# Kernel tuning notes

Hardware: AMD Instinct MI355X
Metric: run time of the kernel (lower is better)

## Reference

```python
import jax, jax.numpy as jnp
import numpy as np


def _fake_quant(x, scale, qmin, qmax):
    # per-tensor int8 fake quant: scale -> round -> clamp -> dequant
    q = jnp.clip(jnp.round(x / scale), qmin, qmax)
    return q * scale


def setup_inputs() -> dict:
    key = jax.random.key(0)
    k1, k2, k3 = jax.random.split(key, 3)
    B, IN, OUT = 4096, 2048, 8192
    x = jax.random.normal(k1, (B, IN), dtype=jnp.float32)
    weight = jax.random.normal(k2, (OUT, IN), dtype=jnp.float32) * 0.02
    bias = jax.random.normal(k3, (OUT,), dtype=jnp.float32) * 0.01
    mul_val = jnp.full((1,), 200.0, dtype=jnp.float32)
    return {"x": x, "weight": weight, "bias": bias, "mul_val": mul_val}


def reference(x, weight, bias, mul_val):
    # Int8ActPerTensorFloat: signed, non-narrow range [-128, 127]
    act_scale = jnp.max(jnp.abs(x)) / 128.0
    xq = _fake_quant(x, act_scale, -128.0, 127.0)
    # Int8WeightPerTensorFloat: signed, narrow range [-127, 127]
    w_scale = jnp.max(jnp.abs(weight)) / 127.0
    wq = _fake_quant(weight, w_scale, -127.0, 127.0)
    # linear: y = xq @ wq.T + b, then elementwise scalar multiply
    y = jnp.einsum("bi,oi->bo", xq, wq) + bias
    return mul_val * y
```

## Files before the change

### kernel.cpp

```cpp
#include <hip/hip_runtime.h>


typedef int v4i  __attribute__((ext_vector_type(4)));
typedef int v16i __attribute__((ext_vector_type(16)));

#define MDIM 4096
#define NDIM 8192
#define KDIM 2048
#define NT   (KDIM / 64)

typedef __attribute__((address_space(1))) void* gas_ptr;
typedef __attribute__((address_space(3))) void* las_ptr;

#define XBLK 1024

__global__ __launch_bounds__(256) void absmax2(const float4* __restrict__ x,
                                               const float4* __restrict__ w,
                                               float* __restrict__ partial) {
    const int tid = threadIdx.x;
    const bool isx = blockIdx.x < XBLK;
    float m0 = 0.0f, m1 = 0.0f;
    if (isx) {
        const size_t base = (size_t)blockIdx.x * 256 + tid;
#pragma unroll
        for (int j = 0; j < 8; j += 2) {
            float4 v0 = x[base + (size_t)j * 262144];
            float4 v1 = x[base + (size_t)(j + 1) * 262144];
            m0 = fmaxf(m0, fmaxf(fmaxf(fabsf(v0.x), fabsf(v0.y)),
                                 fmaxf(fabsf(v0.z), fabsf(v0.w))));
            m1 = fmaxf(m1, fmaxf(fmaxf(fabsf(v1.x), fabsf(v1.y)),
                                 fmaxf(fabsf(v1.z), fabsf(v1.w))));
        }
    } else {
        const size_t base = (size_t)(blockIdx.x - XBLK) * 256 + tid;
#pragma unroll
        for (int j = 0; j < 8; j += 2) {
            float4 v0 = w[base + (size_t)j * 524288];
            float4 v1 = w[base + (size_t)(j + 1) * 524288];
            m0 = fmaxf(m0, fmaxf(fmaxf(fabsf(v0.x), fabsf(v0.y)),
                                 fmaxf(fabsf(v0.z), fabsf(v0.w))));
            m1 = fmaxf(m1, fmaxf(fmaxf(fabsf(v1.x), fabsf(v1.y)),
                                 fmaxf(fabsf(v1.z), fabsf(v1.w))));
        }
    }
    float m = fmaxf(m0, m1);
#pragma unroll
    for (int off = 32; off > 0; off >>= 1)
        m = fmaxf(m, __shfl_xor(m, off, 64));
    __shared__ float wm[4];
    if ((tid & 63) == 0) wm[tid >> 6] = m;
    __syncthreads();
    if (tid == 0)
        partial[blockIdx.x] = fmaxf(fmaxf(wm[0], wm[1]), fmaxf(wm[2], wm[3]));
}

__global__ __launch_bounds__(256) void quant2(const float4* __restrict__ x,
                                              v4i* __restrict__ qxp,
                                              const float4* __restrict__ w,
                                              v4i* __restrict__ qwp,
                                              const float* __restrict__ partial,
                                              unsigned* __restrict__ scales) {
    const int tid = threadIdx.x;
    float gx = 0.0f, gw = 0.0f;
#pragma unroll
    for (int j = 0; j < 4; ++j) gx = fmaxf(gx, partial[tid + j * 256]);
#pragma unroll
    for (int j = 0; j < 8; ++j) gw = fmaxf(gw, partial[XBLK + tid + j * 256]);
#pragma unroll
    for (int off = 32; off > 0; off >>= 1) {
        gx = fmaxf(gx, __shfl_xor(gx, off, 64));
        gw = fmaxf(gw, __shfl_xor(gw, off, 64));
    }
    __shared__ float smx[4], smw[4];
    if ((tid & 63) == 0) { smx[tid >> 6] = gx; smw[tid >> 6] = gw; }
    __syncthreads();
    const float fmx = fmaxf(fmaxf(smx[0], smx[1]), fmaxf(smx[2], smx[3]));
    const float fmw = fmaxf(fmaxf(smw[0], smw[1]), fmaxf(smw[2], smw[3]));
    if (blockIdx.x == 0 && tid == 0) {
        scales[0] = __float_as_uint(fmx);
        scales[1] = __float_as_uint(fmw);
    }
    const float sxs = fmx / 128.0f;
    const float sws = fmw / 127.0f;

    const bool isx = blockIdx.x < XBLK;
    const float4* in = isx ? x : w;
    v4i* outp = isx ? qxp : qwp;
    const int total = isx ? (MDIM * KDIM / 16) : (NDIM * KDIM / 16);
    const int nb = isx ? XBLK : (3072 - XBLK);
    const int b  = isx ? blockIdx.x : (blockIdx.x - XBLK);
    const float s  = isx ? sxs : sws;
    const float lo = isx ? -128.0f : -127.0f;
    for (int idx = b * 256 + tid; idx < total; idx += nb * 256) {
        const int c   = idx & 3;
        const int r   = (idx >> 2) & 255;
        const int kt  = (idx >> 10) & 31;
        const int blk = idx >> 15;
        const float4* src = in + (size_t)(blk * 256 + r) * (KDIM / 4) + kt * 16 + c * 4;
        int q[4];
#pragma unroll
        for (int j = 0; j < 4; ++j) {
            float4 v = src[j];
            int b0 = (int)fminf(fmaxf(rintf(v.x / s), lo), 127.0f);
            int b1 = (int)fminf(fmaxf(rintf(v.y / s), lo), 127.0f);
            int b2 = (int)fminf(fmaxf(rintf(v.z / s), lo), 127.0f);
            int b3 = (int)fminf(fmaxf(rintf(v.w / s), lo), 127.0f);
            q[j] = (b0 & 255) | ((b1 & 255) << 8) | ((b2 & 255) << 16) | (b3 << 24);
        }
        v4i qq; qq[0] = q[0]; qq[1] = q[1]; qq[2] = q[2]; qq[3] = q[3];
        outp[((size_t)(blk * 32 + kt) * 4 + c) * 256 + r] = qq;
    }
}

__global__ __launch_bounds__(512, 2) void gemm_i8(
    const signed char* __restrict__ qxp, const signed char* __restrict__ qwp,
    const float* __restrict__ bias, const float* __restrict__ mulv,
    const unsigned* __restrict__ scales, float* __restrict__ out) {
    __shared__ signed char ldsA[4][16384];
    __shared__ signed char ldsB[4][16384];

    const int t    = threadIdx.x;
    const int lane = t & 63;
    const int ln   = lane & 31;
    const int hi   = lane >> 5;
    const int w    = t >> 6;
    const int wr   = w >> 2;
    const int wc   = w & 3;

    const int orig = blockIdx.x;
    const int xcd  = orig & 7;
    const int idx  = orig >> 3;
    const int bm   = (xcd & 1) * 8 + (idx >> 3);
    const int bn   = (xcd >> 1) * 8 + (idx & 7);

    const signed char* srcA = qxp + (size_t)bm * (32 * 16384);
    const signed char* srcB = qwp + (size_t)bn * (32 * 16384);
    signed char* dA = &ldsA[0][0] + t * 16;
    signed char* dB = &ldsB[0][0] + t * 16;

    auto stage = [&](int buf, int kt) {
        const signed char* sa = srcA + kt * 16384 + t * 16;
        const signed char* sb = srcB + kt * 16384 + t * 16;
        __builtin_amdgcn_global_load_lds((gas_ptr)sa,          (las_ptr)(dA + buf * 16384),        16, 0, 0);
        __builtin_amdgcn_global_load_lds((gas_ptr)(sa + 8192), (las_ptr)(dA + buf * 16384 + 8192), 16, 0, 0);
        __builtin_amdgcn_global_load_lds((gas_ptr)sb,          (las_ptr)(dB + buf * 16384),        16, 0, 0);
        __builtin_amdgcn_global_load_lds((gas_ptr)(sb + 8192), (las_ptr)(dB + buf * 16384 + 8192), 16, 0, 0);
    };

    const int aOff = (wr * 128 + ln) * 16;
    const int bOff = (wc * 64  + ln) * 16;

    v16i acc[4][2];
#pragma unroll
    for (int mt = 0; mt < 4; ++mt)
#pragma unroll
        for (int nt = 0; nt < 2; ++nt)
#pragma unroll
            for (int r = 0; r < 16; ++r) acc[mt][nt][r] = 0;

    auto phase = [&](int kt, int stageKt) {
        const int buf = kt & 3;
        const signed char* A0 = &ldsA[buf][0] + hi * 4096;
        const signed char* B0 = &ldsB[buf][0] + hi * 4096;
        const signed char* A1 = &ldsA[buf][0] + (2 + hi) * 4096;
        const signed char* B1 = &ldsB[buf][0] + (2 + hi) * 4096;

        v4i a0[4], a1[4], b0[2], b1[2];
#pragma unroll
        for (int mt = 0; mt < 4; ++mt) a0[mt] = *(const v4i*)(A0 + aOff + mt * 512);
#pragma unroll
        for (int nt = 0; nt < 2; ++nt) b0[nt] = *(const v4i*)(B0 + bOff + nt * 512);
#pragma unroll
        for (int mt = 0; mt < 4; ++mt) a1[mt] = *(const v4i*)(A1 + aOff + mt * 512);
#pragma unroll
        for (int nt = 0; nt < 2; ++nt) b1[nt] = *(const v4i*)(B1 + bOff + nt * 512);

        if (stageKt < NT) stage(stageKt & 3, stageKt);
        __builtin_amdgcn_s_barrier();
        __builtin_amdgcn_s_setprio(1);
#pragma unroll
        for (int mt = 0; mt < 4; ++mt)
#pragma unroll
            for (int nt = 0; nt < 2; ++nt)
                acc[mt][nt] = __builtin_amdgcn_mfma_i32_32x32x32_i8(
                    a0[mt], b0[nt], acc[mt][nt], 0, 0, 0);
#pragma unroll
        for (int mt = 0; mt < 4; ++mt)
#pragma unroll
            for (int nt = 0; nt < 2; ++nt)
                acc[mt][nt] = __builtin_amdgcn_mfma_i32_32x32x32_i8(
                    a1[mt], b1[nt], acc[mt][nt], 0, 0, 0);
        __builtin_amdgcn_s_setprio(0);
    };

    stage(0, 0);
    stage(1, 1);
    stage(2, 2);
    asm volatile("s_waitcnt vmcnt(4)" ::: "memory");
    __builtin_amdgcn_s_barrier();

    for (int j = 0; j < 15; ++j) {
        phase(2 * j, 2 * j + 3);
        __builtin_amdgcn_s_barrier();
        phase(2 * j + 1, 2 * j + 4);
        asm volatile("s_waitcnt vmcnt(4)" ::: "memory");
        __builtin_amdgcn_s_barrier();
    }
    phase(30, NT);
    asm volatile("s_waitcnt vmcnt(0)" ::: "memory");
    __builtin_amdgcn_s_barrier();
    phase(31, NT);

    const float fm = mulv[0];
    const float fs = fm * (__uint_as_float(scales[0]) / 128.0f)
                        * (__uint_as_float(scales[1]) / 127.0f);
    const int colb = bn * 256 + wc * 64 + ln;
    const int hi4  = hi * 4;
#pragma unroll
    for (int nt = 0; nt < 2; ++nt) {
        const int ocol = colb + nt * 32;
        const float bv = bias[ocol] * fm;
#pragma unroll
        for (int mt = 0; mt < 4; ++mt) {
            float* op = out + (size_t)(bm * 256 + wr * 128 + mt * 32) * NDIM + ocol;
#pragma unroll
            for (int r = 0; r < 16; ++r) {
                const int row = (r & 3) + 8 * (r >> 2) + hi4;
                __builtin_nontemporal_store(fs * (float)acc[mt][nt][r] + bv,
                                            op + (size_t)row * NDIM);
            }
        }
    }
}

extern "C" void kernel_launch(void* const* d_in, const int* in_sizes, int n_in,
                              void* d_out, int out_size, void* d_ws, size_t ws_size,
                              hipStream_t stream) {
    const float4* x    = (const float4*)d_in[0];
    const float4* wgt  = (const float4*)d_in[1];
    const float*  bias = (const float*)d_in[2];
    const float*  mulv = (const float*)d_in[3];
    float* out = (float*)d_out;

    unsigned* scales  = (unsigned*)d_ws;
    float*    partial = (float*)((char*)d_ws + 256);
    signed char* qxp  = (signed char*)d_ws + 256 + 16384;
    signed char* qwp  = qxp + (size_t)MDIM * KDIM;

    absmax2<<<3072, 256, 0, stream>>>(x, wgt, partial);
    quant2<<<3072, 256, 0, stream>>>(x, (v4i*)qxp, wgt, (v4i*)qwp,
                                     partial, scales);
    gemm_i8<<<512, 512, 0, stream>>>(qxp, qwp, bias, mulv, scales, out);
}
```

Before: 122.3 us.

## Double-buffer LDS fragment reads in registers to overlap with MFMA

Restructures the int8 GEMM main loop so the LDS fragment reads for the next k-tile are issued before the MFMAs of the current tile, using two register fragment sets in ping-pong fashion. This also removes the mid-phase barrier, so each k-tile now has one barrier instead of two. The aim is to hide LDS read latency behind matrix-core work and cut synchronisation stalls. The cost is higher VGPR pressure from the extra 12 v4i fragments, which could lower occupancy or cause spills, and it relies on the vmcnt/barrier ordering still protecting the buffer reuse.

```diff
diff --git a/kernel.cpp b/kernel.cpp
--- a/kernel.cpp
+++ b/kernel.cpp
@@ -138,7 +138,9 @@
     signed char* dA = &ldsA[0][0] + t * 16;
     signed char* dB = &ldsB[0][0] + t * 16;
 
-    auto stage = [&](int buf, int kt) {
+    auto stage = [&](int kt) {
+        if (kt >= NT) return;
+        const int buf = kt & 3;
         const signed char* sa = srcA + kt * 16384 + t * 16;
         const signed char* sb = srcB + kt * 16384 + t * 16;
         __builtin_amdgcn_global_load_lds((gas_ptr)sa,          (las_ptr)(dA + buf * 16384),        16, 0, 0);
@@ -150,6 +152,42 @@
     const int aOff = (wr * 128 + ln) * 16;
     const int bOff = (wc * 64  + ln) * 16;
 
+#define READ12(A0, B0, A1, B1, KT) do {                                       \
+        const signed char* _Ab = &ldsA[(KT) & 3][0];                          \
+        const signed char* _Bb = &ldsB[(KT) & 3][0];                          \
+        const signed char* _A0 = _Ab + hi * 4096 + aOff;                      \
+        const signed char* _B0 = _Bb + hi * 4096 + bOff;                      \
+        const signed char* _A1 = _Ab + (2 + hi) * 4096 + aOff;                \
+        const signed char* _B1 = _Bb + (2 + hi) * 4096 + bOff;                \
+        A0[0] = *(const v4i*)(_A0);        A0[1] = *(const v4i*)(_A0 + 512);  \
+        A0[2] = *(const v4i*)(_A0 + 1024); A0[3] = *(const v4i*)(_A0 + 1536); \
+        B0[0] = *(const v4i*)(_B0);        B0[1] = *(const v4i*)(_B0 + 512);  \
+        A1[0] = *(const v4i*)(_A1);        A1[1] = *(const v4i*)(_A1 + 512);  \
+        A1[2] = *(const v4i*)(_A1 + 1024); A1[3] = *(const v4i*)(_A1 + 1536); \
+        B1[0] = *(const v4i*)(_B1);        B1[1] = *(const v4i*)(_B1 + 512);  \
+    } while (0)
+
+#define MFMA16(A0, B0, A1, B1) do {                                           \
+        __builtin_amdgcn_s_setprio(1);                                        \
+        acc[0][0] = __builtin_amdgcn_mfma_i32_32x32x32_i8(A0[0], B0[0], acc[0][0], 0, 0, 0); \
+        acc[0][1] = __builtin_amdgcn_mfma_i32_32x32x32_i8(A0[0], B0[1], acc[0][1], 0, 0, 0); \
+        acc[1][0] = __builtin_amdgcn_mfma_i32_32x32x32_i8(A0[1], B0[0], acc[1][0], 0, 0, 0); \
+        acc[1][1] = __builtin_amdgcn_mfma_i32_32x32x32_i8(A0[1], B0[1], acc[1][1], 0, 0, 0); \
+        acc[2][0] = __builtin_amdgcn_mfma_i32_32x32x32_i8(A0[2], B0[0], acc[2][0], 0, 0, 0); \
+        acc[2][1] = __builtin_amdgcn_mfma_i32_32x32x32_i8(A0[2], B0[1], acc[2][1], 0, 0, 0); \
+        acc[3][0] = __builtin_amdgcn_mfma_i32_32x32x32_i8(A0[3], B0[0], acc[3][0], 0, 0, 0); \
+        acc[3][1] = __builtin_amdgcn_mfma_i32_32x32x32_i8(A0[3], B0[1], acc[3][1], 0, 0, 0); \
+        acc[0][0] = __builtin_amdgcn_mfma_i32_32x32x32_i8(A1[0], B1[0], acc[0][0], 0, 0, 0); \
+        acc[0][1] = __builtin_amdgcn_mfma_i32_32x32x32_i8(A1[0], B1[1], acc[0][1], 0, 0, 0); \
+        acc[1][0] = __builtin_amdgcn_mfma_i32_32x32x32_i8(A1[1], B1[0], acc[1][0], 0, 0, 0); \
+        acc[1][1] = __builtin_amdgcn_mfma_i32_32x32x32_i8(A1[1], B1[1], acc[1][1], 0, 0, 0); \
+        acc[2][0] = __builtin_amdgcn_mfma_i32_32x32x32_i8(A1[2], B1[0], acc[2][0], 0, 0, 0); \
+        acc[2][1] = __builtin_amdgcn_mfma_i32_32x32x32_i8(A1[2], B1[1], acc[2][1], 0, 0, 0); \
+        acc[3][0] = __builtin_amdgcn_mfma_i32_32x32x32_i8(A1[3], B1[0], acc[3][0], 0, 0, 0); \
+        acc[3][1] = __builtin_amdgcn_mfma_i32_32x32x32_i8(A1[3], B1[1], acc[3][1], 0, 0, 0); \
+        __builtin_amdgcn_s_setprio(0);                                        \
+    } while (0)
+
     v16i acc[4][2];
 #pragma unroll
     for (int mt = 0; mt < 4; ++mt)
@@ -158,58 +196,31 @@
 #pragma unroll
             for (int r = 0; r < 16; ++r) acc[mt][nt][r] = 0;
 
-    auto phase = [&](int kt, int stageKt) {
-        const int buf = kt & 3;
-        const signed char* A0 = &ldsA[buf][0] + hi * 4096;
-        const signed char* B0 = &ldsB[buf][0] + hi * 4096;
-        const signed char* A1 = &ldsA[buf][0] + (2 + hi) * 4096;
-        const signed char* B1 = &ldsB[buf][0] + (2 + hi) * 4096;
-
-        v4i a0[4], a1[4], b0[2], b1[2];
-#pragma unroll
-        for (int mt = 0; mt < 4; ++mt) a0[mt] = *(const v4i*)(A0 + aOff + mt * 512);
-#pragma unroll
-        for (int nt = 0; nt < 2; ++nt) b0[nt] = *(const v4i*)(B0 + bOff + nt * 512);
-#pragma unroll
-        for (int mt = 0; mt < 4; ++mt) a1[mt] = *(const v4i*)(A1 + aOff + mt * 512);
-#pragma unroll
-        for (int nt = 0; nt < 2; ++nt) b1[nt] = *(const v4i*)(B1 + bOff + nt * 512);
-
-        if (stageKt < NT) stage(stageKt & 3, stageKt);
-        __builtin_amdgcn_s_barrier();
-        __builtin_amdgcn_s_setprio(1);
-#pragma unroll
-        for (int mt = 0; mt < 4; ++mt)
-#pragma unroll
-            for (int nt = 0; nt < 2; ++nt)
-                acc[mt][nt] = __builtin_amdgcn_mfma_i32_32x32x32_i8(
-                    a0[mt], b0[nt], acc[mt][nt], 0, 0, 0);
-#pragma unroll
-        for (int mt = 0; mt < 4; ++mt)
-#pragma unroll
-            for (int nt = 0; nt < 2; ++nt)
-                acc[mt][nt] = __builtin_amdgcn_mfma_i32_32x32x32_i8(
-                    a1[mt], b1[nt], acc[mt][nt], 0, 0, 0);
-        __builtin_amdgcn_s_setprio(0);
-    };
-
-    stage(0, 0);
-    stage(1, 1);
-    stage(2, 2);
+    v4i f0A0[4], f0B0[2], f0A1[4], f0B1[2];
+    v4i f1A0[4], f1B0[2], f1A1[4], f1B1[2];
+
+    stage(0); stage(1); stage(2);
     asm volatile("s_waitcnt vmcnt(4)" ::: "memory");
     __builtin_amdgcn_s_barrier();
+    READ12(f0A0, f0B0, f0A1, f0B1, 0);
 
     for (int j = 0; j < 15; ++j) {
-        phase(2 * j, 2 * j + 3);
-        __builtin_amdgcn_s_barrier();
-        phase(2 * j + 1, 2 * j + 4);
+        const int kt0 = 2 * j;
+        stage(kt0 + 3);
+        READ12(f1A0, f1B0, f1A1, f1B1, kt0 + 1);
+        MFMA16(f0A0, f0B0, f0A1, f0B1);
         asm volatile("s_waitcnt vmcnt(4)" ::: "memory");
         __builtin_amdgcn_s_barrier();
-    }
-    phase(30, NT);
-    asm volatile("s_waitcnt vmcnt(0)" ::: "memory");
-    __builtin_amdgcn_s_barrier();
-    phase(31, NT);
+        stage(kt0 + 4);
+        READ12(f0A0, f0B0, f0A1, f0B1, kt0 + 2);
+        MFMA16(f1A0, f1B0, f1A1, f1B1);
+        if (j < 14) asm volatile("s_waitcnt vmcnt(4)" ::: "memory");
+        else        asm volatile("s_waitcnt vmcnt(0)" ::: "memory");
+        __builtin_amdgcn_s_barrier();
+    }
+    READ12(f1A0, f1B0, f1A1, f1B1, 31);
+    MFMA16(f0A0, f0B0, f0A1, f0B1);
+    MFMA16(f1A0, f1B0, f1A1, f1B1);
 
     const float fm = mulv[0];
     const float fs = fm * (__uint_as_float(scales[0]) / 128.0f)
@@ -231,6 +242,8 @@
             }
         }
     }
+#undef READ12
+#undef MFMA16
 }
 
 extern "C" void kernel_launch(void* const* d_in, const int* in_sizes, int n_in,
```

Measured after the change: 123.2 us. About the same (+0.7%).

## Shrink GEMM tile to 128x256 with 4 waves and triple-buffered LDS

Applied to the files above, without the earlier changes.

The int8 GEMM moves from 256x256 tiles with 8 waves and a 4-deep LDS ring to 128x256 tiles with 4 waves and a 3-deep ring. The grid grows from 512 to 1024 blocks. The activation pre-pack layout changes to 128-row panels to match. The intent is better load balance across CUs and more resident blocks per CU, since each block uses less LDS. The cost is that every B tile is reloaded twice as often, so arithmetic intensity per byte of LDS traffic drops.

```diff
diff --git a/kernel.cpp b/kernel.cpp
--- a/kernel.cpp
+++ b/kernel.cpp
@@ -92,11 +92,23 @@
     const float s  = isx ? sxs : sws;
     const float lo = isx ? -128.0f : -127.0f;
     for (int idx = b * 256 + tid; idx < total; idx += nb * 256) {
-        const int c   = idx & 3;
-        const int r   = (idx >> 2) & 255;
-        const int kt  = (idx >> 10) & 31;
-        const int blk = idx >> 15;
-        const float4* src = in + (size_t)(blk * 256 + r) * (KDIM / 4) + kt * 16 + c * 4;
+        int c, r, kt, blk, row, oidx;
+        if (isx) {
+            c   = idx & 3;
+            r   = (idx >> 2) & 127;
+            kt  = (idx >> 9) & 31;
+            blk = idx >> 14;
+            row = blk * 128 + r;
+            oidx = ((blk * 32 + kt) * 4 + c) * 128 + r;
+        } else {
+            c   = idx & 3;
+            r   = (idx >> 2) & 255;
+            kt  = (idx >> 10) & 31;
+            blk = idx >> 15;
+            row = blk * 256 + r;
+            oidx = ((blk * 32 + kt) * 4 + c) * 256 + r;
+        }
+        const float4* src = in + (size_t)row * (KDIM / 4) + kt * 16 + c * 4;
         int q[4];
 #pragma unroll
         for (int j = 0; j < 4; ++j) {
@@ -108,47 +120,49 @@
             q[j] = (b0 & 255) | ((b1 & 255) << 8) | ((b2 & 255) << 16) | (b3 << 24);
         }
         v4i qq; qq[0] = q[0]; qq[1] = q[1]; qq[2] = q[2]; qq[3] = q[3];
-        outp[((size_t)(blk * 32 + kt) * 4 + c) * 256 + r] = qq;
-    }
-}
-
-__global__ __launch_bounds__(512, 2) void gemm_i8(
+        outp[oidx] = qq;
+    }
+}
+
+__global__ __launch_bounds__(256, 2) void gemm_i8(
     const signed char* __restrict__ qxp, const signed char* __restrict__ qwp,
     const float* __restrict__ bias, const float* __restrict__ mulv,
     const unsigned* __restrict__ scales, float* __restrict__ out) {
-    __shared__ signed char ldsA[4][16384];
-    __shared__ signed char ldsB[4][16384];
+    __shared__ signed char ldsA[3][8192];
+    __shared__ signed char ldsB[3][16384];
 
     const int t    = threadIdx.x;
     const int lane = t & 63;
     const int ln   = lane & 31;
     const int hi   = lane >> 5;
-    const int w    = t >> 6;
-    const int wr   = w >> 2;
-    const int wc   = w & 3;
+    const int wc   = t >> 6;
 
     const int orig = blockIdx.x;
     const int xcd  = orig & 7;
     const int idx  = orig >> 3;
-    const int bm   = (xcd & 1) * 8 + (idx >> 3);
+    const int bm   = (xcd & 1) * 16 + (idx >> 3);
     const int bn   = (xcd >> 1) * 8 + (idx & 7);
 
-    const signed char* srcA = qxp + (size_t)bm * (32 * 16384);
+    const signed char* srcA = qxp + (size_t)bm * (32 * 8192);
     const signed char* srcB = qwp + (size_t)bn * (32 * 16384);
-    signed char* dA = &ldsA[0][0] + t * 16;
-    signed char* dB = &ldsB[0][0] + t * 16;
-
-    auto stage = [&](int buf, int kt) {
-        const signed char* sa = srcA + kt * 16384 + t * 16;
+    signed char* dA0 = &ldsA[0][0] + t * 16;
+    signed char* dB0 = &ldsB[0][0] + t * 16;
+
+    auto stage = [&](int kt, int buf) {
+        const signed char* sa = srcA + kt * 8192  + t * 16;
         const signed char* sb = srcB + kt * 16384 + t * 16;
-        __builtin_amdgcn_global_load_lds((gas_ptr)sa,          (las_ptr)(dA + buf * 16384),        16, 0, 0);
-        __builtin_amdgcn_global_load_lds((gas_ptr)(sa + 8192), (las_ptr)(dA + buf * 16384 + 8192), 16, 0, 0);
-        __builtin_amdgcn_global_load_lds((gas_ptr)sb,          (las_ptr)(dB + buf * 16384),        16, 0, 0);
-        __builtin_amdgcn_global_load_lds((gas_ptr)(sb + 8192), (las_ptr)(dB + buf * 16384 + 8192), 16, 0, 0);
+        signed char* da = dA0 + buf * 8192;
+        signed char* db = dB0 + buf * 16384;
+        __builtin_amdgcn_global_load_lds((gas_ptr)sa,           (las_ptr)da,            16, 0, 0);
+        __builtin_amdgcn_global_load_lds((gas_ptr)(sa + 4096),  (las_ptr)(da + 4096),   16, 0, 0);
+        __builtin_amdgcn_global_load_lds((gas_ptr)sb,           (las_ptr)db,            16, 0, 0);
+        __builtin_amdgcn_global_load_lds((gas_ptr)(sb + 4096),  (las_ptr)(db + 4096),   16, 0, 0);
+        __builtin_amdgcn_global_load_lds((gas_ptr)(sb + 8192),  (las_ptr)(db + 8192),   16, 0, 0);
+        __builtin_amdgcn_global_load_lds((gas_ptr)(sb + 12288), (las_ptr)(db + 12288),  16, 0, 0);
     };
 
-    const int aOff = (wr * 128 + ln) * 16;
-    const int bOff = (wc * 64  + ln) * 16;
+    const int aOff = ln * 16;
+    const int bOff = (wc * 64 + ln) * 16;
 
     v16i acc[4][2];
 #pragma unroll
@@ -158,25 +172,29 @@
 #pragma unroll
             for (int r = 0; r < 16; ++r) acc[mt][nt][r] = 0;
 
-    auto phase = [&](int kt, int stageKt) {
-        const int buf = kt & 3;
-        const signed char* A0 = &ldsA[buf][0] + hi * 4096;
-        const signed char* B0 = &ldsB[buf][0] + hi * 4096;
-        const signed char* A1 = &ldsA[buf][0] + (2 + hi) * 4096;
-        const signed char* B1 = &ldsB[buf][0] + (2 + hi) * 4096;
+    stage(0, 0);
+    stage(1, 1);
+    asm volatile("s_waitcnt vmcnt(6)" ::: "memory");
+    __builtin_amdgcn_s_barrier();
+
+    int cur = 0, stg = 2;
+    for (int kt = 0; kt < NT; ++kt) {
+        const signed char* Ab = &ldsA[cur][0];
+        const signed char* Bb = &ldsB[cur][0];
 
         v4i a0[4], a1[4], b0[2], b1[2];
 #pragma unroll
-        for (int mt = 0; mt < 4; ++mt) a0[mt] = *(const v4i*)(A0 + aOff + mt * 512);
-#pragma unroll
-        for (int nt = 0; nt < 2; ++nt) b0[nt] = *(const v4i*)(B0 + bOff + nt * 512);
-#pragma unroll
-        for (int mt = 0; mt < 4; ++mt) a1[mt] = *(const v4i*)(A1 + aOff + mt * 512);
-#pragma unroll
-        for (int nt = 0; nt < 2; ++nt) b1[nt] = *(const v4i*)(B1 + bOff + nt * 512);
-
-        if (stageKt < NT) stage(stageKt & 3, stageKt);
+        for (int mt = 0; mt < 4; ++mt) a0[mt] = *(const v4i*)(Ab + hi * 2048 + aOff + mt * 512);
+#pragma unroll
+        for (int nt = 0; nt < 2; ++nt) b0[nt] = *(const v4i*)(Bb + hi * 4096 + bOff + nt * 512);
+#pragma unroll
+        for (int mt = 0; mt < 4; ++mt) a1[mt] = *(const v4i*)(Ab + (2 + hi) * 2048 + aOff + mt * 512);
+#pragma unroll
+        for (int nt = 0; nt < 2; ++nt) b1[nt] = *(const v4i*)(Bb + (2 + hi) * 4096 + bOff + nt * 512);
+
+        if (kt + 2 < NT) stage(kt + 2, stg);
         __builtin_amdgcn_s_barrier();
+
         __builtin_amdgcn_s_setprio(1);
 #pragma unroll
         for (int mt = 0; mt < 4; ++mt)
@@ -191,25 +209,15 @@
                 acc[mt][nt] = __builtin_amdgcn_mfma_i32_32x32x32_i8(
                     a1[mt], b1[nt], acc[mt][nt], 0, 0, 0);
         __builtin_amdgcn_s_setprio(0);
-    };
-
-    stage(0, 0);
-    stage(1, 1);
-    stage(2, 2);
-    asm volatile("s_waitcnt vmcnt(4)" ::: "memory");
-    __builtin_amdgcn_s_barrier();
-
-    for (int j = 0; j < 15; ++j) {
-        phase(2 * j, 2 * j + 3);
-        __builtin_amdgcn_s_barrier();
-        phase(2 * j + 1, 2 * j + 4);
-        asm volatile("s_waitcnt vmcnt(4)" ::: "memory");
-        __builtin_amdgcn_s_barrier();
-    }
-    phase(30, NT);
-    asm volatile("s_waitcnt vmcnt(0)" ::: "memory");
-    __builtin_amdgcn_s_barrier();
-    phase(31, NT);
+
+        if (kt < NT - 1) {
+            if (kt < NT - 2) asm volatile("s_waitcnt vmcnt(6)" ::: "memory");
+            else             asm volatile("s_waitcnt vmcnt(0)" ::: "memory");
+            __builtin_amdgcn_s_barrier();
+        }
+        cur = (cur == 2) ? 0 : cur + 1;
+        stg = (stg == 2) ? 0 : stg + 1;
+    }
 
     const float fm = mulv[0];
     const float fs = fm * (__uint_as_float(scales[0]) / 128.0f)
@@ -222,7 +230,7 @@
         const float bv = bias[ocol] * fm;
 #pragma unroll
         for (int mt = 0; mt < 4; ++mt) {
-            float* op = out + (size_t)(bm * 256 + wr * 128 + mt * 32) * NDIM + ocol;
+            float* op = out + (size_t)(bm * 128 + mt * 32) * NDIM + ocol;
 #pragma unroll
             for (int r = 0; r < 16; ++r) {
                 const int row = (r & 3) + 8 * (r >> 2) + hi4;
@@ -250,5 +258,5 @@
     absmax2<<<3072, 256, 0, stream>>>(x, wgt, partial);
     quant2<<<3072, 256, 0, stream>>>(x, (v4i*)qxp, wgt, (v4i*)qwp,
                                      partial, scales);
-    gemm_i8<<<512, 512, 0, stream>>>(qxp, qwp, bias, mulv, scales, out);
-}
+    gemm_i8<<<1024, 256, 0, stream>>>(qxp, qwp, bias, mulv, scales, out);
+}
```

Result: faster. 119.5 us (-2.3%).
